# Performance work log

Hardware: AMD Instinct MI355X
Metric: run time of the kernel (lower is better)

The kernel has to match this reference:

```python
import jax, jax.numpy as jnp
import numpy as np

N = 50000      # nodes
E = 800000     # edges (before self-loops)
G = 64         # graphs in batch
IN, HID, OUT, H = 128, 64, 64, 4
NEG_SLOPE = 0.2
BN_EPS = 1e-5


def setup_inputs() -> dict:
    key = jax.random.key(0)
    ks = jax.random.split(key, 16)
    s = 0.1
    return {
        "x": jax.random.normal(ks[0], (N, IN), jnp.float32),
        "edge_index": jax.random.randint(ks[1], (2, E), 0, N, dtype=jnp.int64),
        "batch": jnp.sort(jax.random.randint(ks[2], (N,), 0, G, dtype=jnp.int64)),
        "num_graphs": G,
        "W1": jax.random.normal(ks[3], (IN, H * HID), jnp.float32) * s,
        "att_src1": jax.random.normal(ks[4], (H, HID), jnp.float32) * s,
        "att_dst1": jax.random.normal(ks[5], (H, HID), jnp.float32) * s,
        "b1": jnp.zeros((HID,), jnp.float32),
        "W2": jax.random.normal(ks[6], (HID, H * OUT), jnp.float32) * s,
        "att_src2": jax.random.normal(ks[7], (H, OUT), jnp.float32) * s,
        "att_dst2": jax.random.normal(ks[8], (H, OUT), jnp.float32) * s,
        "b2": jnp.zeros((OUT,), jnp.float32),
        "gate_w1": jax.random.normal(ks[9], (OUT, OUT), jnp.float32) * s,
        "gate_b1": jnp.zeros((OUT,), jnp.float32),
        "bn_gamma": jnp.ones((OUT,), jnp.float32),
        "bn_beta": jnp.zeros((OUT,), jnp.float32),
        "gate_w2": jax.random.normal(ks[10], (OUT, 1), jnp.float32) * s,
        "gate_b2": jnp.zeros((1,), jnp.float32),
        "lin_w": jax.random.normal(ks[11], (OUT, 1), jnp.float32) * s,
        "lin_b": jnp.zeros((1,), jnp.float32),
    }


def segment_softmax(e, seg, num_segments):
    # numerically stable softmax over segments (per-destination / per-graph)
    m = jax.ops.segment_max(e, seg, num_segments=num_segments)
    m = jnp.where(jnp.isfinite(m), m, 0.0)
    ex = jnp.exp(e - m[seg])
    den = jax.ops.segment_sum(ex, seg, num_segments=num_segments)
    return ex / (den[seg] + 1e-16)


def gat_conv(x, src, dst, n, W, a_src, a_dst, b, heads, ch):
    h = (x @ W).reshape(n, heads, ch)                 # [N,H,C]
    asrc = jnp.sum(h * a_src, axis=-1)                # [N,H]
    adst = jnp.sum(h * a_dst, axis=-1)                # [N,H]
    e = jax.nn.leaky_relu(asrc[src] + adst[dst], NEG_SLOPE)   # [E',H]
    alpha = segment_softmax(e, dst, n)                # softmax over incoming edges
    out = jax.ops.segment_sum(h[src] * alpha[:, :, None], dst, num_segments=n)
    return jnp.mean(out, axis=1) + b                  # concat=False -> head mean


def reference(x, edge_index, batch, num_graphs, W1, att_src1, att_dst1, b1,
              W2, att_src2, att_dst2, b2, gate_w1, gate_b1, bn_gamma, bn_beta,
              gate_w2, gate_b2, lin_w, lin_b):
    n = x.shape[0]
    loop = jnp.arange(n, dtype=edge_index.dtype)      # PyG add_self_loops default
    src = jnp.concatenate([edge_index[0], loop])
    dst = jnp.concatenate([edge_index[1], loop])

    out = jax.nn.sigmoid(gat_conv(x, src, dst, n, W1, att_src1, att_dst1, b1, H, HID))
    out = jax.nn.sigmoid(gat_conv(out, src, dst, n, W2, att_src2, att_dst2, b2, H, OUT))

    # GlobalAttention pooling; gate_nn = Linear -> BN(eval, rm=0, rv=1) -> ReLU -> Linear
    g = out @ gate_w1 + gate_b1
    g = (g / jnp.sqrt(1.0 + BN_EPS)) * bn_gamma + bn_beta
    g = jax.nn.relu(g) @ gate_w2 + gate_b2            # [N,1]
    gate = segment_softmax(g, batch, num_graphs)      # per-graph softmax
    pooled = jax.ops.segment_sum(gate * out, batch, num_segments=num_graphs)  # [G,OUT]

    return jax.nn.sigmoid(pooled @ lin_w + lin_b)     # [G,1]
```

## Files before the change

### kernel.cpp

```cpp
#include <hip/hip_runtime.h>


constexpr int NN = 50000;
constexpr int EE = 800000;
constexpr int E2 = EE + NN;
constexpr int NG = 64;
constexpr float NEG = 0.2f;
constexpr int MT = NN / 16;
constexpr int SLOTS = 64;
constexpr int CH = 16;
constexpr int GB = (MT + 3) / 4;
constexpr int EDGE_NB = (E2 + 255) / 256;
constexpr int ZERO_NB = (NN + 255) / 256;

using bf16x8 = __attribute__((ext_vector_type(8))) __bf16;
using f32x4  = __attribute__((ext_vector_type(4))) float;
using f32x2  = __attribute__((ext_vector_type(2))) float;

__device__ __forceinline__ float wred(float v) {
#pragma unroll
  for (int o = 32; o; o >>= 1) v += __shfl_down(v, o);
  return v;
}
__device__ __forceinline__ float sigmoidf(float v) { return 1.f / (1.f + __expf(-v)); }
__device__ __forceinline__ float lrelu(float v) { return fmaxf(v, NEG * v); }
__device__ __forceinline__ unsigned short f2b(float f) {
  union { float f; unsigned u; } v; v.f = f;
  unsigned r = v.u + 0x7fff + ((v.u >> 16) & 1);
  return (unsigned short)(r >> 16);
}
__device__ __forceinline__ float b2f(unsigned short b) {
  union { unsigned u; float f; } v; v.u = ((unsigned)b) << 16;
  return v.f;
}

__global__ void prep_kernel(const float* __restrict__ W1, const float* __restrict__ W2,
                            const float* __restrict__ gw1, const float* __restrict__ gamma,
                            const int* __restrict__ batch, int* __restrict__ cnt,
                            unsigned short* __restrict__ W1b, unsigned short* __restrict__ W2b,
                            unsigned short* __restrict__ Bg, int* __restrict__ goffs) {
  int b = blockIdx.x;
  if (b < ZERO_NB) {
    int i = b * 256 + threadIdx.x;
    if (i < NN) cnt[i] = 0;
    return;
  }
  if (b < ZERO_NB + 128) {
    int idx = (b - ZERO_NB) * 256 + threadIdx.x;
    int j = idx & 7, lane = (idx >> 3) & 63, rest = idx >> 9;
    int kc = rest & 3, ntile = rest >> 2;
    W1b[idx] = f2b(W1[(kc * 32 + (lane >> 4) * 8 + j) * 256 + ntile * 16 + (lane & 15)]);
    return;
  }
  if (b < ZERO_NB + 192) {
    int idx = (b - ZERO_NB - 128) * 256 + threadIdx.x;
    int j = idx & 7, lane = (idx >> 3) & 63, rest = idx >> 9;
    int kc = rest & 1, ntile = rest >> 1;
    W2b[idx] = f2b(W2[(kc * 32 + (lane >> 4) * 8 + j) * 256 + ntile * 16 + (lane & 15)]);
    return;
  }
  if (b < ZERO_NB + 208) {
    int idx = (b - ZERO_NB - 192) * 256 + threadIdx.x;
    int j = idx & 7, lane = (idx >> 3) & 63, rest = idx >> 9;
    int kc = rest & 1, nt = rest >> 1;
    int k = kc * 32 + (lane >> 4) * 8 + j;
    int n = nt * 16 + (lane & 15);
    Bg[idx] = f2b(gw1[k * 64 + n] * gamma[n] * rsqrtf(1.f + 1e-5f));
    return;
  }
  int g = threadIdx.x;
  if (g <= NG) {
    int lo = 0, hi = NN;
    while (lo < hi) {
      int mid = (lo + hi) >> 1;
      if (batch[mid] < g) lo = mid + 1; else hi = mid;
    }
    goffs[g] = lo;
  }
}

template <int K, bool A32>
__device__ __forceinline__ void gemm_body(int mt, int lane,
                                          const void* __restrict__ A_raw,
                                          const unsigned short* __restrict__ Bp,
                                          unsigned char* __restrict__ C8,
                                          const float* __restrict__ att_s,
                                          const float* __restrict__ att_d,
                                          float* __restrict__ asrc,
                                          float* __restrict__ adst) {
  constexpr int KC = K / 32;
  int m0 = mt * 16;
  int q = lane >> 4, r = lane & 15;
  f32x4 acc[16] = {};
#pragma unroll
  for (int kc = 0; kc < KC; ++kc) {
    bf16x8 a;
    if constexpr (A32) {
      const float* Arow = (const float*)A_raw + (size_t)(m0 + r) * K + q * 8 + kc * 32;
      float4 f0 = *(const float4*)Arow;
      float4 f1 = *(const float4*)(Arow + 4);
      union { bf16x8 v; unsigned short s[8]; } u;
      u.s[0] = f2b(f0.x); u.s[1] = f2b(f0.y); u.s[2] = f2b(f0.z); u.s[3] = f2b(f0.w);
      u.s[4] = f2b(f1.x); u.s[5] = f2b(f1.y); u.s[6] = f2b(f1.z); u.s[7] = f2b(f1.w);
      a = u.v;
    } else {
      a = *(const bf16x8*)((const unsigned short*)A_raw +
                           (size_t)(m0 + r) * K + q * 8 + kc * 32);
    }
#pragma unroll
    for (int nt = 0; nt < 16; ++nt) {
      bf16x8 b = *(const bf16x8*)&Bp[(((size_t)nt * KC + kc) * 64 + lane) * 8];
      acc[nt] = __builtin_amdgcn_mfma_f32_16x16x32_bf16(a, b, acc[nt], 0, 0, 0);
    }
  }
#pragma unroll
  for (int nt = 0; nt < 16; ++nt) {
    unsigned col = nt * 16 + r;
#pragma unroll
    for (int reg = 0; reg < 4; ++reg) {
      unsigned row = m0 + q * 4 + reg;
      int p = __builtin_amdgcn_cvt_pk_fp8_f32(acc[nt][reg], 0.f, 0, false);
      C8[row * 256u + col] = (unsigned char)(p & 0xff);
    }
  }
  float ps[4][4] = {}, pd[4][4] = {};
#pragma unroll
  for (int head = 0; head < 4; ++head) {
#pragma unroll
    for (int i = 0; i < 4; ++i) {
      float sv = att_s[head * 64 + i * 16 + r];
      float dv = att_d[head * 64 + i * 16 + r];
#pragma unroll
      for (int reg = 0; reg < 4; ++reg) {
        ps[head][reg] += acc[head * 4 + i][reg] * sv;
        pd[head][reg] += acc[head * 4 + i][reg] * dv;
      }
    }
  }
#pragma unroll
  for (int head = 0; head < 4; ++head)
#pragma unroll
    for (int reg = 0; reg < 4; ++reg)
#pragma unroll
      for (int o = 1; o < 16; o <<= 1) {
        ps[head][reg] += __shfl_xor(ps[head][reg], o);
        pd[head][reg] += __shfl_xor(pd[head][reg], o);
      }
  if (r == 0) {
#pragma unroll
    for (int reg = 0; reg < 4; ++reg) {
      int row = m0 + q * 4 + reg;
#pragma unroll
      for (int head = 0; head < 4; ++head) {
        asrc[row * 4 + head] = ps[head][reg];
        adst[row * 4 + head] = pd[head][reg];
      }
    }
  }
}

__global__ void gemm1_build_kernel(const float* __restrict__ x,
                                   const unsigned short* __restrict__ W1b,
                                   unsigned char* __restrict__ C8,
                                   const float* __restrict__ att_s,
                                   const float* __restrict__ att_d,
                                   float* __restrict__ asrc, float* __restrict__ adst,
                                   const int* __restrict__ ei, int* __restrict__ cnt,
                                   int* __restrict__ csr_src) {
  int b = blockIdx.x;
  if (b < GB) {
    int wave = threadIdx.x >> 6, lane = threadIdx.x & 63;
    int mt = b * 4 + wave;
    if (mt >= MT) return;
    gemm_body<128, true>(mt, lane, x, W1b, C8, att_s, att_d, asrc, adst);
    return;
  }
  int e = (b - GB) * 256 + threadIdx.x;
  if (e >= E2) return;
  int src, dst;
  if (e < EE) { src = ei[e]; dst = ei[EE + e]; }
  else { src = dst = e - EE; }
  int rank = atomicAdd(&cnt[dst], 1);
  if (rank < SLOTS) csr_src[(unsigned)dst * SLOTS + rank] = src;
}

__global__ void gemm2_kernel(const unsigned short* __restrict__ out1b,
                             const unsigned short* __restrict__ W2b,
                             unsigned char* __restrict__ C8,
                             const float* __restrict__ att_s,
                             const float* __restrict__ att_d,
                             float* __restrict__ asrc, float* __restrict__ adst) {
  int wave = threadIdx.x >> 6, lane = threadIdx.x & 63;
  int mt = blockIdx.x * 4 + wave;
  if (mt >= MT) return;
  gemm_body<64, false>(mt, lane, out1b, W2b, C8, att_s, att_d, asrc, adst);
}

__global__ void aggregate_kernel(const unsigned char* __restrict__ h8,
                                 const float* __restrict__ asrc,
                                 const float* __restrict__ adst,
                                 const int* __restrict__ cnt,
                                 const int* __restrict__ csr_src,
                                 const float* __restrict__ bias,
                                 unsigned short* __restrict__ outb) {
  int wave = threadIdx.x >> 6, lane = threadIdx.x & 63;
  int node = blockIdx.x * 4 + wave;
  if (node >= NN) return;
  int deg = min(cnt[node], SLOTS);
  int hgrp = lane >> 4;
  int hb = lane & 48;
  float adh = adst[node * 4 + hgrp];
  int src_all = csr_src[(unsigned)node * SLOTS + lane];
  float wreg[4];
  float den = 0.f;
#pragma unroll
  for (int i = 0; i < 4; ++i) {
    int slot = i * 16 + (lane & 15);
    int s = __shfl(src_all, slot);
    bool valid = slot < deg;
    float xv = asrc[(unsigned)(valid ? s : 0) * 4 + hgrp];
    float w = __expf(lrelu(xv + adh));
    wreg[i] = valid ? w : 0.f;
    den += wreg[i];
  }
#pragma unroll
  for (int o = 1; o < 16; o <<= 1) den += __shfl_xor(den, o);
  const unsigned char* hp = h8 + (unsigned)lane * 4;
  f32x2 a01 = {0.f, 0.f}, a23 = {0.f, 0.f};
  int e = 0;
#pragma unroll
  for (int i = 0; i < 4; ++i) {
    if (e >= deg) break;
    float wcur = wreg[i];
    int bound = min(deg, (i + 1) * 16);
    for (; e + 3 < bound; e += 4) {
      int s0 = __shfl(src_all, e),     s1 = __shfl(src_all, e + 1);
      int s2 = __shfl(src_all, e + 2), s3 = __shfl(src_all, e + 3);
      float w0 = __shfl(wcur, ((e)     & 15) | hb);
      float w1 = __shfl(wcur, ((e + 1) & 15) | hb);
      float w2 = __shfl(wcur, ((e + 2) & 15) | hb);
      float w3 = __shfl(wcur, ((e + 3) & 15) | hb);
      unsigned d0 = *(const unsigned*)(hp + ((unsigned)s0 << 8));
      unsigned d1 = *(const unsigned*)(hp + ((unsigned)s1 << 8));
      unsigned d2 = *(const unsigned*)(hp + ((unsigned)s2 << 8));
      unsigned d3 = *(const unsigned*)(hp + ((unsigned)s3 << 8));
      f32x2 l0 = __builtin_amdgcn_cvt_pk_f32_fp8(d0, false), u0 = __builtin_amdgcn_cvt_pk_f32_fp8(d0, true);
      f32x2 l1 = __builtin_amdgcn_cvt_pk_f32_fp8(d1, false), u1 = __builtin_amdgcn_cvt_pk_f32_fp8(d1, true);
      f32x2 l2 = __builtin_amdgcn_cvt_pk_f32_fp8(d2, false), u2 = __builtin_amdgcn_cvt_pk_f32_fp8(d2, true);
      f32x2 l3 = __builtin_amdgcn_cvt_pk_f32_fp8(d3, false), u3 = __builtin_amdgcn_cvt_pk_f32_fp8(d3, true);
      a01 += l0 * w0; a23 += u0 * w0;
      a01 += l1 * w1; a23 += u1 * w1;
      a01 += l2 * w2; a23 += u2 * w2;
      a01 += l3 * w3; a23 += u3 * w3;
    }
    for (; e < bound; ++e) {
      int s0 = __shfl(src_all, e);
      float w0 = __shfl(wcur, (e & 15) | hb);
      unsigned d0 = *(const unsigned*)(hp + ((unsigned)s0 << 8));
      f32x2 l0 = __builtin_amdgcn_cvt_pk_f32_fp8(d0, false), u0 = __builtin_amdgcn_cvt_pk_f32_fp8(d0, true);
      a01 += l0 * w0; a23 += u0 * w0;
    }
  }
  float inv = 1.f / (den + 1e-16f);
  float r0 = a01.x * inv, r1 = a01.y * inv, r2 = a23.x * inv, r3 = a23.y * inv;
  r0 += __shfl_xor(r0, 16); r0 += __shfl_xor(r0, 32);
  r1 += __shfl_xor(r1, 16); r1 += __shfl_xor(r1, 32);
  r2 += __shfl_xor(r2, 16); r2 += __shfl_xor(r2, 32);
  r3 += __shfl_xor(r3, 16); r3 += __shfl_xor(r3, 32);
  if (lane < 16) {
    float4 bv = *(const float4*)&bias[lane * 4];
    ushort4 o;
    o.x = f2b(sigmoidf(0.25f * r0 + bv.x));
    o.y = f2b(sigmoidf(0.25f * r1 + bv.y));
    o.z = f2b(sigmoidf(0.25f * r2 + bv.z));
    o.w = f2b(sigmoidf(0.25f * r3 + bv.w));
    *(ushort4*)&outb[(size_t)node * 64 + lane * 4] = o;
  }
}

__global__ void gate_mfma_kernel(const unsigned short* __restrict__ out2b,
                                 const unsigned short* __restrict__ Bg,
                                 const float* __restrict__ gb1, const float* __restrict__ gamma,
                                 const float* __restrict__ beta, const float* __restrict__ gw2,
                                 const float* __restrict__ gb2, float* __restrict__ g) {
  int wave = threadIdx.x >> 6, lane = threadIdx.x & 63;
  int mt = blockIdx.x * 4 + wave;
  if (mt >= MT) return;
  int m0 = mt * 16;
  int q = lane >> 4, r = lane & 15;
  f32x4 acc[4] = {};
  const unsigned short* Arow = out2b + (size_t)(m0 + r) * 64 + q * 8;
#pragma unroll
  for (int kc = 0; kc < 2; ++kc) {
    bf16x8 a = *(const bf16x8*)(Arow + kc * 32);
#pragma unroll
    for (int nt = 0; nt < 4; ++nt) {
      bf16x8 b = *(const bf16x8*)&Bg[(((size_t)nt * 2 + kc) * 64 + lane) * 8];
      acc[nt] = __builtin_amdgcn_mfma_f32_16x16x32_bf16(a, b, acc[nt], 0, 0, 0);
    }
  }
  const float s = rsqrtf(1.f + 1e-5f);
  float sum[4] = {0.f, 0.f, 0.f, 0.f};
#pragma unroll
  for (int nt = 0; nt < 4; ++nt) {
    int col = nt * 16 + r;
    float off = gb1[col] * gamma[col] * s + beta[col];
    float w2 = gw2[col];
#pragma unroll
    for (int reg = 0; reg < 4; ++reg)
      sum[reg] += fmaxf(acc[nt][reg] + off, 0.f) * w2;
  }
#pragma unroll
  for (int reg = 0; reg < 4; ++reg)
#pragma unroll
    for (int o = 1; o < 16; o <<= 1) sum[reg] += __shfl_xor(sum[reg], o);
  if (r == 0) {
    float gb2v = gb2[0];
#pragma unroll
    for (int reg = 0; reg < 4; ++reg) g[m0 + q * 4 + reg] = sum[reg] + gb2v;
  }
}

__global__ void pool_partial_kernel(const float* __restrict__ g, const int* __restrict__ goffs,
                                    const unsigned short* __restrict__ out2b,
                                    float* __restrict__ part_acc,
                                    float* __restrict__ part_den) {
  int b = blockIdx.x, j = blockIdx.y;
  int beg = goffs[b], end = goffs[b + 1];
  int chunk = (end - beg + CH - 1) / CH;
  int cb = beg + j * chunk;
  int ce = min(end, cb + chunk);
  int lane = threadIdx.x & 63, wave = threadIdx.x >> 6;
  float acc = 0.f, den = 0.f;
  for (int n = cb + wave; n < ce; n += 4) {
    float ex = __expf(g[n]);
    acc += ex * b2f(out2b[(size_t)n * 64 + lane]);
    den += ex;
  }
  __shared__ float sacc[4][64];
  __shared__ float sden[4];
  sacc[wave][lane] = acc;
  if (lane == 0) sden[wave] = den;
  __syncthreads();
  if (wave == 0) {
    float a = sacc[0][lane] + sacc[1][lane] + sacc[2][lane] + sacc[3][lane];
    part_acc[((size_t)b * CH + j) * 64 + lane] = a;
    if (lane == 0) part_den[b * CH + j] = sden[0] + sden[1] + sden[2] + sden[3];
  }
}

__global__ void pool_final_kernel(const float* __restrict__ part_acc,
                                  const float* __restrict__ part_den,
                                  const float* __restrict__ lw, const float* __restrict__ lb,
                                  float* __restrict__ out) {
  int b = blockIdx.x, lane = threadIdx.x;
  float a = 0.f;
#pragma unroll
  for (int j = 0; j < CH; ++j) a += part_acc[((size_t)b * CH + j) * 64 + lane];
  float den = (lane < CH) ? part_den[b * CH + lane] : 0.f;
  den = wred(den);
  den = __shfl(den, 0);
  float p = a / (den + 1e-16f);
  float v = wred(p * lw[lane]);
  if (lane == 0) out[b] = sigmoidf(v + lb[0]);
}

extern "C" void kernel_launch(void* const* d_in, const int* in_sizes, int n_in,
                              void* d_out, int out_size, void* d_ws, size_t ws_size,
                              hipStream_t stream) {
  const float* x    = (const float*)d_in[0];
  const int*   ei   = (const int*)d_in[1];
  const int*   batch= (const int*)d_in[2];
  const float* W1   = (const float*)d_in[4];
  const float* as1  = (const float*)d_in[5];
  const float* ad1  = (const float*)d_in[6];
  const float* b1   = (const float*)d_in[7];
  const float* W2   = (const float*)d_in[8];
  const float* as2  = (const float*)d_in[9];
  const float* ad2  = (const float*)d_in[10];
  const float* b2   = (const float*)d_in[11];
  const float* gw1  = (const float*)d_in[12];
  const float* gb1  = (const float*)d_in[13];
  const float* gamma= (const float*)d_in[14];
  const float* beta = (const float*)d_in[15];
  const float* gw2  = (const float*)d_in[16];
  const float* gb2  = (const float*)d_in[17];
  const float* lw   = (const float*)d_in[18];
  const float* lb   = (const float*)d_in[19];
  float* out = (float*)d_out;

  char* ws = (char*)d_ws;
  size_t off = 0;
  auto alloc = [&](size_t bytes) -> void* {
    void* p = ws + off;
    off = (off + bytes + 255) & ~(size_t)255;
    return p;
  };
  unsigned short* W1b    = (unsigned short*)alloc((size_t)128 * 256 * 2);
  unsigned short* W2b    = (unsigned short*)alloc((size_t)64 * 256 * 2);
  unsigned short* Bg     = (unsigned short*)alloc((size_t)64 * 64 * 2);
  unsigned char*  h8     = (unsigned char*)alloc((size_t)NN * 256);
  unsigned short* out1b  = (unsigned short*)alloc((size_t)NN * 64 * 2);
  unsigned short* out2b  = (unsigned short*)alloc((size_t)NN * 64 * 2);
  float*    asrc    = (float*)alloc((size_t)NN * 4 * 4);
  float*    adst    = (float*)alloc((size_t)NN * 4 * 4);
  float*    g       = (float*)alloc((size_t)NN * 4);
  int*      cnt     = (int*)alloc((size_t)NN * 4);
  int*      csr_src = (int*)alloc((size_t)NN * SLOTS * 4);
  int*      goffs   = (int*)alloc((size_t)(NG + 1) * 4);
  float*    pacc    = (float*)alloc((size_t)NG * CH * 64 * 4);
  float*    pden    = (float*)alloc((size_t)NG * CH * 4);

  const int nodeBlocks = (NN + 3) / 4;

  prep_kernel<<<ZERO_NB + 209, 256, 0, stream>>>(W1, W2, gw1, gamma, batch, cnt,
                                                 W1b, W2b, Bg, goffs);

  gemm1_build_kernel<<<GB + EDGE_NB, 256, 0, stream>>>(x, W1b, h8, as1, ad1, asrc, adst,
                                                       ei, cnt, csr_src);
  aggregate_kernel<<<nodeBlocks, 256, 0, stream>>>(h8, asrc, adst, cnt, csr_src, b1, out1b);

  gemm2_kernel<<<GB, 256, 0, stream>>>(out1b, W2b, h8, as2, ad2, asrc, adst);
  aggregate_kernel<<<nodeBlocks, 256, 0, stream>>>(h8, asrc, adst, cnt, csr_src, b2, out2b);

  gate_mfma_kernel<<<GB, 256, 0, stream>>>(out2b, Bg, gb1, gamma, beta, gw2, gb2, g);
  pool_partial_kernel<<<dim3(NG, CH), 256, 0, stream>>>(g, goffs, out2b, pacc, pden);
  pool_final_kernel<<<NG, 64, 0, stream>>>(pacc, pden, lw, lb, out);
}
```

Before: 270.5 us.

## Fuse gate MLP into pooling kernel and partition CSR build by destination range

The separate gate MFMA kernel is removed; each pooling wave now computes the gate logits for its 16-row tiles with MFMA and consumes them directly, so the g buffer and one kernel launch go away. The edge CSR build launches 8x as many blocks, and each block only handles edges whose destination falls in its one-eighth node range. That clustering aims to improve atomic and scatter locality on cnt and csr_src. In exchange, the edge indices are read eight times over, and the pool kernel repeats small reads of the gate weights.

```diff
diff --git a/kernel.cpp b/kernel.cpp
--- a/kernel.cpp
+++ b/kernel.cpp
@@ -12,6 +12,7 @@
 constexpr int GB = (MT + 3) / 4;
 constexpr int EDGE_NB = (E2 + 255) / 256;
 constexpr int ZERO_NB = (NN + 255) / 256;
+constexpr int RNG = NN / 8;
 
 using bf16x8 = __attribute__((ext_vector_type(8))) __bf16;
 using f32x4  = __attribute__((ext_vector_type(4))) float;
@@ -175,11 +176,13 @@
     gemm_body<128, true>(mt, lane, x, W1b, C8, att_s, att_d, asrc, adst);
     return;
   }
-  int e = (b - GB) * 256 + threadIdx.x;
+  int b2 = b - GB;
+  int range = b2 & 7;
+  int e = (b2 >> 3) * 256 + threadIdx.x;
   if (e >= E2) return;
-  int src, dst;
-  if (e < EE) { src = ei[e]; dst = ei[EE + e]; }
-  else { src = dst = e - EE; }
+  int dst = (e < EE) ? ei[EE + e] : (e - EE);
+  if (dst / RNG != range) return;
+  int src = (e < EE) ? ei[e] : dst;
   int rank = atomicAdd(&cnt[dst], 1);
   if (rank < SLOTS) csr_src[(unsigned)dst * SLOTS + rank] = src;
 }
@@ -278,51 +281,14 @@
   }
 }
 
-__global__ void gate_mfma_kernel(const unsigned short* __restrict__ out2b,
-                                 const unsigned short* __restrict__ Bg,
-                                 const float* __restrict__ gb1, const float* __restrict__ gamma,
-                                 const float* __restrict__ beta, const float* __restrict__ gw2,
-                                 const float* __restrict__ gb2, float* __restrict__ g) {
-  int wave = threadIdx.x >> 6, lane = threadIdx.x & 63;
-  int mt = blockIdx.x * 4 + wave;
-  if (mt >= MT) return;
-  int m0 = mt * 16;
-  int q = lane >> 4, r = lane & 15;
-  f32x4 acc[4] = {};
-  const unsigned short* Arow = out2b + (size_t)(m0 + r) * 64 + q * 8;
-#pragma unroll
-  for (int kc = 0; kc < 2; ++kc) {
-    bf16x8 a = *(const bf16x8*)(Arow + kc * 32);
-#pragma unroll
-    for (int nt = 0; nt < 4; ++nt) {
-      bf16x8 b = *(const bf16x8*)&Bg[(((size_t)nt * 2 + kc) * 64 + lane) * 8];
-      acc[nt] = __builtin_amdgcn_mfma_f32_16x16x32_bf16(a, b, acc[nt], 0, 0, 0);
-    }
-  }
-  const float s = rsqrtf(1.f + 1e-5f);
-  float sum[4] = {0.f, 0.f, 0.f, 0.f};
-#pragma unroll
-  for (int nt = 0; nt < 4; ++nt) {
-    int col = nt * 16 + r;
-    float off = gb1[col] * gamma[col] * s + beta[col];
-    float w2 = gw2[col];
-#pragma unroll
-    for (int reg = 0; reg < 4; ++reg)
-      sum[reg] += fmaxf(acc[nt][reg] + off, 0.f) * w2;
-  }
-#pragma unroll
-  for (int reg = 0; reg < 4; ++reg)
-#pragma unroll
-    for (int o = 1; o < 16; o <<= 1) sum[reg] += __shfl_xor(sum[reg], o);
-  if (r == 0) {
-    float gb2v = gb2[0];
-#pragma unroll
-    for (int reg = 0; reg < 4; ++reg) g[m0 + q * 4 + reg] = sum[reg] + gb2v;
-  }
-}
-
-__global__ void pool_partial_kernel(const float* __restrict__ g, const int* __restrict__ goffs,
+__global__ void pool_partial_kernel(const int* __restrict__ goffs,
                                     const unsigned short* __restrict__ out2b,
+                                    const unsigned short* __restrict__ Bg,
+                                    const float* __restrict__ gb1,
+                                    const float* __restrict__ gamma,
+                                    const float* __restrict__ beta,
+                                    const float* __restrict__ gw2,
+                                    const float* __restrict__ gb2,
                                     float* __restrict__ part_acc,
                                     float* __restrict__ part_den) {
   int b = blockIdx.x, j = blockIdx.y;
@@ -331,15 +297,56 @@
   int cb = beg + j * chunk;
   int ce = min(end, cb + chunk);
   int lane = threadIdx.x & 63, wave = threadIdx.x >> 6;
-  float acc = 0.f, den = 0.f;
-  for (int n = cb + wave; n < ce; n += 4) {
-    float ex = __expf(g[n]);
-    acc += ex * b2f(out2b[(size_t)n * 64 + lane]);
-    den += ex;
+  int q = lane >> 4, r = lane & 15;
+  const float s = rsqrtf(1.f + 1e-5f);
+  float gb2v = gb2[0];
+  float accv = 0.f, den = 0.f;
+  for (int n0 = cb + wave * 16; n0 < ce; n0 += 64) {
+    f32x4 acc[4] = {};
+    int row = n0 + r;
+    if (row >= NN) row = NN - 1;
+    const unsigned short* Arow = out2b + (size_t)row * 64 + q * 8;
+#pragma unroll
+    for (int kc = 0; kc < 2; ++kc) {
+      bf16x8 a = *(const bf16x8*)(Arow + kc * 32);
+#pragma unroll
+      for (int nt = 0; nt < 4; ++nt) {
+        bf16x8 b8 = *(const bf16x8*)&Bg[(((size_t)nt * 2 + kc) * 64 + lane) * 8];
+        acc[nt] = __builtin_amdgcn_mfma_f32_16x16x32_bf16(a, b8, acc[nt], 0, 0, 0);
+      }
+    }
+    float sum[4] = {0.f, 0.f, 0.f, 0.f};
+#pragma unroll
+    for (int nt = 0; nt < 4; ++nt) {
+      int col = nt * 16 + r;
+      float off = gb1[col] * gamma[col] * s + beta[col];
+      float w2 = gw2[col];
+#pragma unroll
+      for (int reg = 0; reg < 4; ++reg)
+        sum[reg] += fmaxf(acc[nt][reg] + off, 0.f) * w2;
+    }
+#pragma unroll
+    for (int reg = 0; reg < 4; ++reg)
+#pragma unroll
+      for (int o = 1; o < 16; o <<= 1) sum[reg] += __shfl_xor(sum[reg], o);
+    float gx[4];
+#pragma unroll
+    for (int reg = 0; reg < 4; ++reg) {
+      int n = n0 + q * 4 + reg;
+      gx[reg] = (n < ce) ? __expf(sum[reg] + gb2v) : 0.f;
+    }
+#pragma unroll
+    for (int t = 0; t < 16; ++t) {
+      int n = n0 + t;
+      if (n >= ce) break;
+      float gv = __shfl(gx[t & 3], (t >> 2) << 4);
+      accv += gv * b2f(out2b[(size_t)n * 64 + lane]);
+      den += gv;
+    }
   }
   __shared__ float sacc[4][64];
   __shared__ float sden[4];
-  sacc[wave][lane] = acc;
+  sacc[wave][lane] = accv;
   if (lane == 0) sden[wave] = den;
   __syncthreads();
   if (wave == 0) {
@@ -404,7 +411,6 @@
   unsigned short* out2b  = (unsigned short*)alloc((size_t)NN * 64 * 2);
   float*    asrc    = (float*)alloc((size_t)NN * 4 * 4);
   float*    adst    = (float*)alloc((size_t)NN * 4 * 4);
-  float*    g       = (float*)alloc((size_t)NN * 4);
   int*      cnt     = (int*)alloc((size_t)NN * 4);
   int*      csr_src = (int*)alloc((size_t)NN * SLOTS * 4);
   int*      goffs   = (int*)alloc((size_t)(NG + 1) * 4);
@@ -416,14 +422,14 @@
   prep_kernel<<<ZERO_NB + 209, 256, 0, stream>>>(W1, W2, gw1, gamma, batch, cnt,
                                                  W1b, W2b, Bg, goffs);
 
-  gemm1_build_kernel<<<GB + EDGE_NB, 256, 0, stream>>>(x, W1b, h8, as1, ad1, asrc, adst,
-                                                       ei, cnt, csr_src);
+  gemm1_build_kernel<<<GB + 8 * EDGE_NB, 256, 0, stream>>>(x, W1b, h8, as1, ad1, asrc, adst,
+                                                           ei, cnt, csr_src);
   aggregate_kernel<<<nodeBlocks, 256, 0, stream>>>(h8, asrc, adst, cnt, csr_src, b1, out1b);
 
   gemm2_kernel<<<GB, 256, 0, stream>>>(out1b, W2b, h8, as2, ad2, asrc, adst);
   aggregate_kernel<<<nodeBlocks, 256, 0, stream>>>(h8, asrc, adst, cnt, csr_src, b2, out2b);
 
-  gate_mfma_kernel<<<GB, 256, 0, stream>>>(out2b, Bg, gb1, gamma, beta, gw2, gb2, g);
-  pool_partial_kernel<<<dim3(NG, CH), 256, 0, stream>>>(g, goffs, out2b, pacc, pden);
+  pool_partial_kernel<<<dim3(NG, CH), 256, 0, stream>>>(goffs, out2b, Bg, gb1, gamma, beta,
+                                                        gw2, gb2, pacc, pden);
   pool_final_kernel<<<NG, 64, 0, stream>>>(pacc, pden, lw, lb, out);
 }
```

Measured after the change: 273.8 us. No clear change (+1.2%).
